# Kernel optimization log

Measured on AMD Instinct MI355X. Metric: run time of the kernel, lower is better.

Reference implementation:

```python
import math
import jax, jax.numpy as jnp
import numpy as np

B, T, D_MODEL, N_HEADS = 2, 2048, 1024, 16
HEAD_DIM = D_MODEL // N_HEADS  # 64


def setup_inputs() -> dict:
    key = jax.random.key(0)
    k1, k2, k3, k4, k5 = jax.random.split(key, 5)
    x = jax.random.normal(k1, (B, T, D_MODEL), dtype=jnp.float32)
    init = 0.02
    Wq = jax.random.normal(k2, (D_MODEL, D_MODEL), dtype=jnp.float32) * init
    Wk = jax.random.normal(k3, (D_MODEL, D_MODEL), dtype=jnp.float32) * init
    Wv = jax.random.normal(k4, (D_MODEL, D_MODEL), dtype=jnp.float32) * init
    Wo = jax.random.normal(k5, (D_MODEL, D_MODEL), dtype=jnp.float32) * init
    # causal mask, broadcastable over (B, H): 1 = keep, 0 = masked
    mask = jnp.tril(jnp.ones((T, T), dtype=jnp.int32))[None, None, :, :]
    return {"x": x, "Wq": Wq, "Wk": Wk, "Wv": Wv, "Wo": Wo, "mask": mask}


def ternary_weight(W):
    # BitNet-b1.58 style ternary quantization with straight-through estimator
    scale = jnp.mean(jnp.abs(W))
    Wt = jnp.round(jnp.clip(W / (scale + 1e-8), -1.0, 1.0)) * scale
    return W + jax.lax.stop_gradient(Wt - W)


def rope_cos_sin(seq_len, dim):
    inv_freq = 1.0 / (10000.0 ** (jnp.arange(0, dim, 2, dtype=jnp.float32) / dim))
    freqs = jnp.outer(jnp.arange(seq_len, dtype=jnp.float32), inv_freq)  # [T, dim/2]
    emb = jnp.concatenate([freqs, freqs], axis=-1)  # [T, dim]
    return jnp.cos(emb)[None, None, :, :], jnp.sin(emb)[None, None, :, :]


def rotate_half(x):
    h = x.shape[-1] // 2
    return jnp.concatenate([-x[..., h:], x[..., :h]], axis=-1)


def reference(x, Wq, Wk, Wv, Wo, mask):
    Bb, Tt, C = x.shape
    H, D = N_HEADS, HEAD_DIM
    # ternary-quantized projections (bias-free)
    q = (x @ ternary_weight(Wq).T).reshape(Bb, Tt, H, D).transpose(0, 2, 1, 3)
    k = (x @ ternary_weight(Wk).T).reshape(Bb, Tt, H, D).transpose(0, 2, 1, 3)
    v = (x @ ternary_weight(Wv).T).reshape(Bb, Tt, H, D).transpose(0, 2, 1, 3)
    cos, sin = rope_cos_sin(Tt, D)  # [1,1,T,D]
    q = q * cos + rotate_half(q) * sin
    k = k * cos + rotate_half(k) * sin
    att = jnp.einsum("bhqd,bhkd->bhqk", q, k) / math.sqrt(D)
    att = jnp.where(mask == 0, -jnp.inf, att)
    att = jax.nn.softmax(att, axis=-1)  # dropout omitted (eval mode, p effectively 0)
    y = jnp.einsum("bhqk,bhkd->bhqd", att, v)
    y = y.transpose(0, 2, 1, 3).reshape(Bb, Tt, C)
    return y @ ternary_weight(Wo).T
```

## Files before the change

kernel.cpp:

```cpp
#include <hip/hip_runtime.h>
#include <math.h>

using bf16x8  = __attribute__((ext_vector_type(8))) __bf16;
using floatx4 = __attribute__((ext_vector_type(4))) float;
using ushortx8 = __attribute__((ext_vector_type(8))) unsigned short;
using ushortx4 = __attribute__((ext_vector_type(4))) unsigned short;
typedef unsigned short u16;

__device__ __forceinline__ float bf2f(u16 u) {
  unsigned int x = ((unsigned int)u) << 16;
  return __builtin_bit_cast(float, x);
}
__device__ __forceinline__ u16 f2bf(float f) {
  unsigned int x = __builtin_bit_cast(unsigned int, f);
  x += 0x7FFFu + ((x >> 16) & 1u);
  return (u16)(x >> 16);
}
__device__ __forceinline__ float fexp2(float x) { return __builtin_amdgcn_exp2f(x); }
__device__ __forceinline__ unsigned cvtpk(float lo, float hi) {
  unsigned r;
  asm("v_cvt_pk_bf16_f32 %0, %1, %2" : "=v"(r) : "v"(lo), "v"(hi));
  return r;
}
__device__ __forceinline__ float scale_of(const float* __restrict__ partials, int w) {
  float s = 0.f;
  for (int i = 0; i < 64; ++i) s += partials[w * 64 + i];
  return s * (1.f / 1048576.f);
}

#define GLDS16(SRC, DST)                                                        \
  __builtin_amdgcn_global_load_lds((const __attribute__((address_space(1))) void*)(SRC), \
                                   (__attribute__((address_space(3))) void*)(DST), 16, 0, 0)

__global__ __launch_bounds__(256) void prep_kernel(const float* __restrict__ x, u16* __restrict__ xb,
                                                   const float* W0, const float* W1,
                                                   const float* W2, const float* W3,
                                                   float* partials) {
  __shared__ float red[256];
  int tid = threadIdx.x;
  if (blockIdx.x < 2048) {
    int g = (blockIdx.x * 256 + tid) * 8;
    float4 a = *(const float4*)(x + g);
    float4 b = *(const float4*)(x + g + 4);
    ushortx8 o;
    o[0] = f2bf(a.x); o[1] = f2bf(a.y); o[2] = f2bf(a.z); o[3] = f2bf(a.w);
    o[4] = f2bf(b.x); o[5] = f2bf(b.y); o[6] = f2bf(b.z); o[7] = f2bf(b.w);
    *(ushortx8*)(xb + g) = o;
    return;
  }
  int idx = blockIdx.x - 2048;
  int bx = idx & 63, w = idx >> 6;
  const float* W = (w == 0) ? W0 : (w == 1) ? W1 : (w == 2) ? W2 : W3;
  int base = bx * 16384 + tid;
  float s = 0.f;
#pragma unroll
  for (int i = 0; i < 64; ++i) s += fabsf(W[base + i * 256]);
  red[tid] = s;
  __syncthreads();
  for (int off = 128; off > 0; off >>= 1) {
    if (tid < off) red[tid] += red[tid + off];
    __syncthreads();
  }
  if (tid == 0) partials[w * 64 + bx] = red[0];
}

__global__ __launch_bounds__(256) void quant_kernel(const float* W0, const float* W1,
                                                    const float* W2, const float* W3,
                                                    const float* partials, u16* Wt) {
  int w = blockIdx.y;
  const float* W = (w == 0) ? W0 : (w == 1) ? W1 : (w == 2) ? W2 : W3;
  u16* O = Wt + (size_t)w * (1u << 20);
  float s = scale_of(partials, w) + 1e-8f;
  int e = (blockIdx.x * 256 + threadIdx.x) * 4;
  float4 v = *(const float4*)(W + e);
  ushortx4 o;
  o[0] = f2bf(rintf(fminf(fmaxf(v.x / s, -1.f), 1.f)));
  o[1] = f2bf(rintf(fminf(fmaxf(v.y / s, -1.f), 1.f)));
  o[2] = f2bf(rintf(fminf(fmaxf(v.z / s, -1.f), 1.f)));
  o[3] = f2bf(rintf(fminf(fmaxf(v.w / s, -1.f), 1.f)));
  *(ushortx4*)(O + e) = o;
}

__global__ __launch_bounds__(256) void gemm_qkv(const u16* __restrict__ A, const u16* __restrict__ Wt,
                                                u16* __restrict__ QKV, u16* __restrict__ vt,
                                                const float* __restrict__ partials) {
  const int K = 1024;
  __shared__ __align__(16) u16 As[128][64];
  __shared__ __align__(16) u16 Bs[64][64];
  int tid = threadIdx.x;
  int wave = tid >> 6, lane = tid & 63;
  int quad = lane >> 4, l16 = lane & 15;
  int bm = blockIdx.x * 128;
  int bnc = blockIdx.y * 64;
  int mat = bnc >> 10, bn = bnc & 1023;
  int wm = wave * 32;
  floatx4 acc[2][4] = {};
  int scol = ((lane & 7) ^ ((lane >> 3) & 7)) * 8;
  const u16* ga = A  + (size_t)(bm + wave * 32 + (lane >> 3)) * K + scol;
  const u16* gb = Wt + (size_t)(bnc + wave * 16 + (lane >> 3)) * K + scol;
  int rx = (l16 & 7);
  for (int k0 = 0; k0 < K; k0 += 64) {
    __syncthreads();
#pragma unroll
    for (int i = 0; i < 4; ++i)
      GLDS16(ga + (size_t)i * 8 * K + k0, &As[wave * 32 + i * 8][0]);
#pragma unroll
    for (int i = 0; i < 2; ++i)
      GLDS16(gb + (size_t)i * 8 * K + k0, &Bs[wave * 16 + i * 8][0]);
    __syncthreads();
#pragma unroll
    for (int kk = 0; kk < 64; kk += 32) {
      int col = (((kk >> 3) + quad) ^ rx) * 8;
      bf16x8 a[2], b[4];
#pragma unroll
      for (int i = 0; i < 2; ++i)
        a[i] = __builtin_bit_cast(bf16x8, *(const ushortx8*)&As[wm + i * 16 + l16][col]);
#pragma unroll
      for (int j = 0; j < 4; ++j)
        b[j] = __builtin_bit_cast(bf16x8, *(const ushortx8*)&Bs[j * 16 + l16][col]);
#pragma unroll
      for (int i = 0; i < 2; ++i)
#pragma unroll
        for (int j = 0; j < 4; ++j)
          acc[i][j] = __builtin_amdgcn_mfma_f32_16x16x32_bf16(a[i], b[j], acc[i][j], 0, 0, 0);
    }
  }
  float sc = scale_of(partials, mat);
  if (mat < 2) {
    u16* outp = QKV + (size_t)mat * (4u << 20);
    float qs = (mat == 0) ? 0.125f * 1.4426950408889634f : 1.0f;
    float inv0 = exp2f(-(float)l16 * (13.287712379549449f / 32.f));
    float inv1 = exp2f(-(float)(16 + l16) * (13.287712379549449f / 32.f));
#pragma unroll
    for (int i = 0; i < 2; ++i)
#pragma unroll
      for (int rg = 0; rg < 4; ++rg) {
        int row = bm + wm + i * 16 + quad * 4 + rg;
        float tf = (float)(row & 2047);
#pragma unroll
        for (int j = 0; j < 2; ++j) {
          float ang = tf * (j ? inv1 : inv0);
          float s = __sinf(ang), c = __cosf(ang);
          float v1 = acc[i][j][rg] * sc, v2 = acc[i][j + 2][rg] * sc;
          int col = bn + j * 16 + l16;
          outp[(size_t)row * 1024 + col]      = f2bf((v1 * c - v2 * s) * qs);
          outp[(size_t)row * 1024 + col + 32] = f2bf((v2 * c + v1 * s) * qs);
        }
      }
  } else {
    int h = bn >> 6;
#pragma unroll
    for (int i = 0; i < 2; ++i) {
      int row0 = bm + wm + i * 16 + quad * 4;
      int b = row0 >> 11, t0 = row0 & 2047;
#pragma unroll
      for (int j = 0; j < 4; ++j) {
        int d = j * 16 + l16;
        ushortx4 o;
#pragma unroll
        for (int rg = 0; rg < 4; ++rg) o[rg] = f2bf(acc[i][j][rg] * sc);
        *(ushortx4*)(vt + (size_t)((b * 16 + h) * 64 + d) * 2048 + t0) = o;
      }
    }
  }
}

__global__ __launch_bounds__(256) void gemm_out(const u16* __restrict__ A, const u16* __restrict__ B,
                                                float* __restrict__ C, const float* __restrict__ partials) {
  const int K = 1024, N = 1024;
  __shared__ __align__(16) u16 As[128][64];
  __shared__ __align__(16) u16 Bs[64][64];
  int tid = threadIdx.x;
  int wave = tid >> 6, lane = tid & 63;
  int quad = lane >> 4, l16 = lane & 15;
  int bm = blockIdx.x * 128, bn = blockIdx.y * 64;
  int wm = (wave >> 1) * 64, wn = (wave & 1) * 32;
  floatx4 acc[4][2] = {};
  int scol = ((lane & 7) ^ ((lane >> 3) & 7)) * 8;
  const u16* ga = A + (size_t)(bm + wave * 32 + (lane >> 3)) * K + scol;
  const u16* gb = B + (size_t)(bn + wave * 16 + (lane >> 3)) * K + scol;
  int rx = (l16 & 7);
  for (int k0 = 0; k0 < K; k0 += 64) {
    __syncthreads();
#pragma unroll
    for (int i = 0; i < 4; ++i)
      GLDS16(ga + (size_t)i * 8 * K + k0, &As[wave * 32 + i * 8][0]);
#pragma unroll
    for (int i = 0; i < 2; ++i)
      GLDS16(gb + (size_t)i * 8 * K + k0, &Bs[wave * 16 + i * 8][0]);
    __syncthreads();
#pragma unroll
    for (int kk = 0; kk < 64; kk += 32) {
      int col = (((kk >> 3) + quad) ^ rx) * 8;
      bf16x8 a[4], b[2];
#pragma unroll
      for (int i = 0; i < 4; ++i)
        a[i] = __builtin_bit_cast(bf16x8, *(const ushortx8*)&As[wm + i * 16 + l16][col]);
#pragma unroll
      for (int j = 0; j < 2; ++j)
        b[j] = __builtin_bit_cast(bf16x8, *(const ushortx8*)&Bs[wn + j * 16 + l16][col]);
#pragma unroll
      for (int i = 0; i < 4; ++i)
#pragma unroll
        for (int j = 0; j < 2; ++j)
          acc[i][j] = __builtin_amdgcn_mfma_f32_16x16x32_bf16(a[i], b[j], acc[i][j], 0, 0, 0);
    }
  }
  float sc = scale_of(partials, 3);
#pragma unroll
  for (int i = 0; i < 4; ++i)
#pragma unroll
    for (int j = 0; j < 2; ++j)
#pragma unroll
      for (int rg = 0; rg < 4; ++rg) {
        int row = bm + wm + i * 16 + quad * 4 + rg;
        int col = bn + wn + j * 16 + l16;
        C[(size_t)row * N + col] = acc[i][j][rg] * sc;
      }
}

__global__ __launch_bounds__(256, 3) void attn_kernel(const u16* __restrict__ q, const u16* __restrict__ k,
                                                      const u16* __restrict__ vt, u16* __restrict__ y) {
  __shared__ __align__(16) u16 Ks[2][64][64];
  __shared__ __align__(16) u16 Vt[2][64][64];
  __shared__ __align__(16) u16 Ps[4][16][72];
  const int T = 2048, C = 1024;
  int tid = threadIdx.x;
  int wave = tid >> 6, lane = tid & 63;
  int quad = lane >> 4, l16 = lane & 15;
  int p = blockIdx.y;
  int bh = blockIdx.x;
  int b = bh >> 4, h = bh & 15;
  int wq[2];
  wq[0] = p * 64 + wave * 16;
  wq[1] = (31 - p) * 64 + wave * 16;
  int dt[2] = {p, 31 - p};
  int nkt = 32 - p;

  bf16x8 bq[2][2];
#pragma unroll
  for (int g = 0; g < 2; ++g) {
    const u16* gq = q + (size_t)(b * T + wq[g] + l16) * C + h * 64 + quad * 8;
    bq[g][0] = __builtin_bit_cast(bf16x8, *(const ushortx8*)(gq));
    bq[g][1] = __builtin_bit_cast(bf16x8, *(const ushortx8*)(gq + 32));
  }

  ushortx8 onesu;
#pragma unroll
  for (int j = 0; j < 8; ++j) onesu[j] = 0x3F80;
  bf16x8 bones = __builtin_bit_cast(bf16x8, onesu);

  int grow = lane >> 3;
  int gchk = ((lane & 7) ^ grow) * 8;
  const u16* kbase = k  + (size_t)(b * T + grow) * C + h * 64 + gchk;
  const u16* vbase = vt + (size_t)(bh * 64 + grow) * 2048 + gchk;

#define STAGE_KV(BB, KT)                                                                     \
  do {                                                                                       \
    _Pragma("unroll")                                                                        \
    for (int i_ = 0; i_ < 2; ++i_) {                                                         \
      int rb_ = (wave + 4 * i_) * 8;                                                         \
      GLDS16(kbase + (size_t)((KT) * 64 + rb_) * C, &Ks[BB][rb_][0]);                        \
      GLDS16(vbase + (size_t)rb_ * 2048 + (KT) * 64, &Vt[BB][rb_][0]);                       \
    }                                                                                        \
  } while (0)

  floatx4 o[2][5] = {};

  STAGE_KV(0, 0);
  __syncthreads();

  int rxk = l16 & 7;

  for (int kt = 0; kt < nkt; ++kt) {
    int cur = kt & 1;
    if (kt + 1 < nkt) STAGE_KV(cur ^ 1, kt + 1);

    bool act[2] = {kt <= dt[0], true};

    floatx4 sacc[2][4] = {};
#pragma unroll
    for (int nt = 0; nt < 4; ++nt) {
      bf16x8 ak0 = __builtin_bit_cast(bf16x8, *(const ushortx8*)&Ks[cur][nt * 16 + l16][(quad ^ rxk) * 8]);
      bf16x8 ak1 = __builtin_bit_cast(bf16x8, *(const ushortx8*)&Ks[cur][nt * 16 + l16][((quad | 4) ^ rxk) * 8]);
#pragma unroll
      for (int g = 0; g < 2; ++g)
        if (act[g]) {
          sacc[g][nt] = __builtin_amdgcn_mfma_f32_16x16x32_bf16(ak0, bq[g][0], sacc[g][nt], 0, 0, 0);
          sacc[g][nt] = __builtin_amdgcn_mfma_f32_16x16x32_bf16(ak1, bq[g][1], sacc[g][nt], 0, 0, 0);
        }
    }

    bf16x8 ap[2][2];
#pragma unroll
    for (int g = 0; g < 2; ++g)
      if (act[g]) {
        if (kt == dt[g]) {
          int qg = wq[g] + l16;
#pragma unroll
          for (int nt = 0; nt < 4; ++nt)
#pragma unroll
            for (int rg = 0; rg < 4; ++rg)
              if (kt * 64 + nt * 16 + quad * 4 + rg > qg) sacc[g][nt][rg] = -__builtin_inff();
        }
#pragma unroll
        for (int nt = 0; nt < 4; ++nt) {
          float p0 = fexp2(sacc[g][nt][0]);
          float p1 = fexp2(sacc[g][nt][1]);
          float p2 = fexp2(sacc[g][nt][2]);
          float p3 = fexp2(sacc[g][nt][3]);
          unsigned lo = cvtpk(p0, p1);
          unsigned hi = cvtpk(p2, p3);
          *(uint2*)&Ps[wave][l16][nt * 16 + quad * 4] = make_uint2(lo, hi);
        }
        ap[g][0] = __builtin_bit_cast(bf16x8, *(const ushortx8*)&Ps[wave][l16][quad * 8]);
        ap[g][1] = __builtin_bit_cast(bf16x8, *(const ushortx8*)&Ps[wave][l16][32 + quad * 8]);
      }

#pragma unroll
    for (int nt = 0; nt < 4; ++nt) {
      bf16x8 bv0 = __builtin_bit_cast(bf16x8, *(const ushortx8*)&Vt[cur][nt * 16 + l16][(quad ^ rxk) * 8]);
      bf16x8 bv1 = __builtin_bit_cast(bf16x8, *(const ushortx8*)&Vt[cur][nt * 16 + l16][((quad | 4) ^ rxk) * 8]);
#pragma unroll
      for (int g = 0; g < 2; ++g)
        if (act[g]) {
          o[g][nt] = __builtin_amdgcn_mfma_f32_16x16x32_bf16(ap[g][0], bv0, o[g][nt], 0, 0, 0);
          o[g][nt] = __builtin_amdgcn_mfma_f32_16x16x32_bf16(ap[g][1], bv1, o[g][nt], 0, 0, 0);
        }
    }
#pragma unroll
    for (int g = 0; g < 2; ++g)
      if (act[g]) {
        o[g][4] = __builtin_amdgcn_mfma_f32_16x16x32_bf16(ap[g][0], bones, o[g][4], 0, 0, 0);
        o[g][4] = __builtin_amdgcn_mfma_f32_16x16x32_bf16(ap[g][1], bones, o[g][4], 0, 0, 0);
      }

    __syncthreads();
  }
#undef STAGE_KV

#pragma unroll
  for (int g = 0; g < 2; ++g) {
    float inv[4];
#pragma unroll
    for (int rg = 0; rg < 4; ++rg) inv[rg] = __builtin_amdgcn_rcpf(o[g][4][rg]);
#pragma unroll
    for (int nt = 0; nt < 4; ++nt)
#pragma unroll
      for (int rg = 0; rg < 4; ++rg) {
        int qg = wq[g] + quad * 4 + rg;
        int col = h * 64 + nt * 16 + l16;
        y[(size_t)(b * T + qg) * C + col] = f2bf(o[g][nt][rg] * inv[rg]);
      }
  }
}

extern "C" void kernel_launch(void* const* d_in, const int* in_sizes, int n_in,
                              void* d_out, int out_size, void* d_ws, size_t ws_size,
                              hipStream_t stream) {
  const float* x  = (const float*)d_in[0];
  const float* Wq = (const float*)d_in[1];
  const float* Wk = (const float*)d_in[2];
  const float* Wv = (const float*)d_in[3];
  const float* Wo = (const float*)d_in[4];

  char* ws = (char*)d_ws;
  float* partials = (float*)ws;
  u16* Wt  = (u16*)(ws + 4096);
  u16* xb  = (u16*)(ws + 4096 + (size_t)(8u << 20));
  u16* qb  = xb + (4u << 20);
  u16* kb  = qb + (4u << 20);
  u16* vtb = kb + (4u << 20);
  u16* yb  = vtb + (4u << 20);
  float* out = (float*)d_out;

  prep_kernel<<<2304, 256, 0, stream>>>(x, xb, Wq, Wk, Wv, Wo, partials);
  quant_kernel<<<dim3(1024, 4), 256, 0, stream>>>(Wq, Wk, Wv, Wo, partials, Wt);

  gemm_qkv<<<dim3(32, 48), 256, 0, stream>>>(xb, Wt, qb, vtb, partials);
  attn_kernel<<<dim3(32, 16), 256, 0, stream>>>(qb, kb, vtb, yb);
  gemm_out<<<dim3(32, 16), 256, 0, stream>>>(yb, Wt + 3 * (1u << 20), out, partials);
}
```

Baseline: 185.4 us.

## Double-buffer LDS tiles in QKV GEMM with prefetch two stages ahead

Converts the QKV projection GEMM's shared-memory tiles to a two-slot ring. Global-to-LDS loads for tile k+2 are issued right after tile k is consumed, and explicit vmcnt waits plus raw s_barriers replace the __syncthreads pairs. This is meant to hide global load latency behind MFMA work. It doubles LDS use, which may reduce occupancy, and relies on hand-counted vmcnt values being correct.

```diff
diff --git a/kernel.cpp b/kernel.cpp
--- a/kernel.cpp
+++ b/kernel.cpp
@@ -85,8 +85,8 @@
                                                 u16* __restrict__ QKV, u16* __restrict__ vt,
                                                 const float* __restrict__ partials) {
   const int K = 1024;
-  __shared__ __align__(16) u16 As[128][64];
-  __shared__ __align__(16) u16 Bs[64][64];
+  __shared__ __align__(16) u16 As[2][128][64];
+  __shared__ __align__(16) u16 Bs[2][64][64];
   int tid = threadIdx.x;
   int wave = tid >> 6, lane = tid & 63;
   int quad = lane >> 4, l16 = lane & 15;
@@ -99,32 +99,48 @@
   const u16* ga = A  + (size_t)(bm + wave * 32 + (lane >> 3)) * K + scol;
   const u16* gb = Wt + (size_t)(bnc + wave * 16 + (lane >> 3)) * K + scol;
   int rx = (l16 & 7);
+
+#define STAGE_AB(BB, KO)                                                        \
+  do {                                                                          \
+    _Pragma("unroll")                                                           \
+    for (int i_ = 0; i_ < 4; ++i_)                                              \
+      GLDS16(ga + (size_t)i_ * 8 * K + (KO), &As[BB][wave * 32 + i_ * 8][0]);   \
+    _Pragma("unroll")                                                           \
+    for (int i_ = 0; i_ < 2; ++i_)                                              \
+      GLDS16(gb + (size_t)i_ * 8 * K + (KO), &Bs[BB][wave * 16 + i_ * 8][0]);   \
+  } while (0)
+
+  STAGE_AB(0, 0);
+  STAGE_AB(1, 64);
   for (int k0 = 0; k0 < K; k0 += 64) {
-    __syncthreads();
-#pragma unroll
-    for (int i = 0; i < 4; ++i)
-      GLDS16(ga + (size_t)i * 8 * K + k0, &As[wave * 32 + i * 8][0]);
-#pragma unroll
-    for (int i = 0; i < 2; ++i)
-      GLDS16(gb + (size_t)i * 8 * K + k0, &Bs[wave * 16 + i * 8][0]);
-    __syncthreads();
+    int bb = (k0 >> 6) & 1;
+    if (k0 == K - 64) asm volatile("s_waitcnt vmcnt(0)" ::: "memory");
+    else              asm volatile("s_waitcnt vmcnt(6)" ::: "memory");
+    __builtin_amdgcn_sched_barrier(0);
+    __builtin_amdgcn_s_barrier();
+    __builtin_amdgcn_sched_barrier(0);
 #pragma unroll
     for (int kk = 0; kk < 64; kk += 32) {
       int col = (((kk >> 3) + quad) ^ rx) * 8;
       bf16x8 a[2], b[4];
 #pragma unroll
       for (int i = 0; i < 2; ++i)
-        a[i] = __builtin_bit_cast(bf16x8, *(const ushortx8*)&As[wm + i * 16 + l16][col]);
+        a[i] = __builtin_bit_cast(bf16x8, *(const ushortx8*)&As[bb][wm + i * 16 + l16][col]);
 #pragma unroll
       for (int j = 0; j < 4; ++j)
-        b[j] = __builtin_bit_cast(bf16x8, *(const ushortx8*)&Bs[j * 16 + l16][col]);
+        b[j] = __builtin_bit_cast(bf16x8, *(const ushortx8*)&Bs[bb][j * 16 + l16][col]);
 #pragma unroll
       for (int i = 0; i < 2; ++i)
 #pragma unroll
         for (int j = 0; j < 4; ++j)
           acc[i][j] = __builtin_amdgcn_mfma_f32_16x16x32_bf16(a[i], b[j], acc[i][j], 0, 0, 0);
     }
-  }
+    __builtin_amdgcn_s_barrier();
+    __builtin_amdgcn_sched_barrier(0);
+    if (k0 + 128 < K) STAGE_AB(bb, k0 + 128);
+  }
+#undef STAGE_AB
+
   float sc = scale_of(partials, mat);
   if (mat < 2) {
     u16* outp = QKV + (size_t)mat * (4u << 20);
```

After: 187.6 us. About the same (+1.2%).
